# Kernel optimization log

Measured on AMD Instinct MI355X. Metric: run time of the kernel, lower is better.

The kernel has to match this reference:

```python
import jax, jax.numpy as jnp
import numpy as np

K = 3  # kernel_size, padding=1, stride=1 (same-size unfold)


def unfold3x3(x):
    """x: [B, C, H, W] -> [B, C, 9, H, W], matching torch.nn.Unfold(3, padding=1)
    channel-major / row-major kernel-position ordering."""
    H, W = x.shape[2], x.shape[3]
    xp = jnp.pad(x, ((0, 0), (0, 0), (1, 1), (1, 1)))
    patches = [xp[:, :, i:i + H, j:j + W] for i in range(K) for j in range(K)]
    return jnp.stack(patches, axis=2)


def setup_inputs() -> dict:
    key = jax.random.key(0)
    k1, k2, k3, k4 = jax.random.split(key, 4)
    B, CF, H, W = 2, 64, 64, 2048
    coord_C = 3
    out_Cs = (16, 64)  # out_Cs[-1] == CF
    features = jax.random.normal(k1, (B, CF, H, W), dtype=jnp.float32)
    coord = jax.random.normal(k2, (B, coord_C, H, W), dtype=jnp.float32)
    w0 = jax.random.normal(k3, (out_Cs[0], coord_C), dtype=jnp.float32) * 0.1
    w1 = jax.random.normal(k4, (out_Cs[1], out_Cs[0]), dtype=jnp.float32) * 0.1
    return {"features": features, "coord": coord, "w0": w0, "w1": w1}


def reference(features, coord, w0, w1):
    # --- gather 3x3 coord neighborhood, relative coords ---
    coord_sample = unfold3x3(coord)                    # [B, 3, 9, H, W]
    center = coord[:, :, None]                         # [B, 3, 1, H, W]
    rel = coord_sample - center
    rel = jnp.where(center == -1.0, 0.0, rel)          # zero invalid centers
    # --- weight-generation MLP: 1x1 convs over channel dim, per pixel & neighbor ---
    h = jnp.einsum('oc,bcnhw->bonhw', w0, rel)         # [B, 16, 9, H, W]
    h = jnp.einsum('oc,bcnhw->bonhw', w1, h)           # [B, 64, 9, H, W]
    weights = jax.nn.relu(h)                           # ReLU only after last layer
    # --- gather 3x3 feature neighborhood, weighted combine ---
    feat_sample = unfold3x3(features)                  # [B, CF, 9, H, W]
    out = feat_sample * weights                        # [B, CF, 9, H, W]
    B, CF, KK, H, W = out.shape
    return out.reshape(B, CF * KK, H, W)               # [B, CF*9, H, W]
```

## Files before the change

### kernel.cpp

```cpp
#include <hip/hip_runtime.h>

#define BB   2
#define CF_  64
#define CC   3
#define HH   64
#define WW   2048
#define HWs  (HH * WW)
#define KK   9
#define CFS  4
#define CFT  (CF_ / CFS)
#define PX   2

typedef float f2 __attribute__((ext_vector_type(2)));

__global__ __launch_bounds__(256) void fused_unfold_mlp_kernel(
    const float* __restrict__ feat,
    const float* __restrict__ coord,
    const float* __restrict__ w0,
    const float* __restrict__ w1,
    float* __restrict__ out)
{
    __shared__ float Msh[CFT * CC];

    const int t = threadIdx.x;
    const int p = blockIdx.x * 256 + t;
    const int q = p >> 17;

    if (t < CFT * CC) {
        const int o = t / CC, c = t - o * CC;
        const int og = q * CFT + o;
        float acc = 0.f;
#pragma unroll
        for (int k = 0; k < 16; k++)
            acc = fmaf(w1[og * 16 + k], w0[k * CC + c], acc);
        Msh[t] = acc;
    }
    __syncthreads();

    float ms[CFT * CC];
#pragma unroll
    for (int j = 0; j < CFT * CC; j++)
        ms[j] = __uint_as_float(__builtin_amdgcn_readfirstlane(__float_as_uint(Msh[j])));

    const int w2  = p & (WW / 2 - 1);
    const int w0p = w2 * 2;
    const int h   = (p >> 10) & (HH - 1);
    const int b   = (p >> 16) & (BB - 1);

    const float* __restrict__ cb = coord + (size_t)b * CC * HWs;
    float rel[PX][CC][KK];
#pragma unroll
    for (int px = 0; px < PX; px++) {
        const int w = w0p + px;
        float center[CC];
#pragma unroll
        for (int c = 0; c < CC; c++)
            center[c] = cb[c * HWs + h * WW + w];
#pragma unroll
        for (int n = 0; n < KK; n++) {
            const int di = n / 3 - 1, dj = n % 3 - 1;
            const int hh = h + di, ww = w + dj;
            const bool v = (hh >= 0) && (hh < HH) && (ww >= 0) && (ww < WW);
            const int off = (v ? hh : h) * WW + (v ? ww : w);
#pragma unroll
            for (int c = 0; c < CC; c++) {
                const float r = cb[c * HWs + off] - center[c];
                rel[px][c][n] = (v && center[c] != -1.0f) ? r : 0.0f;
            }
        }
    }

    int rows[3];
    rows[0] = (h > 0      ? h - 1 : 0     ) * WW;
    rows[1] = h * WW;
    rows[2] = (h < HH - 1 ? h + 1 : HH - 1) * WW;
    const int cm1 = (w0p > 0)      ? (w0p - 1) : 0;
    const int cp2 = (w0p + 2 < WW) ? (w0p + 2) : (WW - 1);

    const float* __restrict__ fb = feat + (size_t)b * CF_ * HWs;
    const int cfbase = q * CFT;
    f2* __restrict__ ob2 = (f2*)(out
        + (size_t)(b * CF_ * KK + cfbase * KK) * HWs + (size_t)h * WW + w0p);

    auto loadF = [&](float* buf, int cfi) {
        const float* fc = fb + (size_t)(cfbase + cfi) * HWs;
#pragma unroll
        for (int r = 0; r < 3; r++) {
            const float* rp = fc + rows[r];
            buf[r * 4 + 0] = rp[cm1];
            const f2 mid   = *(const f2*)(rp + w0p);
            buf[r * 4 + 1] = mid[0];
            buf[r * 4 + 2] = mid[1];
            buf[r * 4 + 3] = rp[cp2];
        }
    };

    auto computeStore = [&](const float* fv, int i) {
        const float m0 = ms[i * CC + 0], m1 = ms[i * CC + 1], m2 = ms[i * CC + 2];
#pragma unroll
        for (int n = 0; n < KK; n++) {
            const int r = n / 3, j = n % 3;
            float wg0 = fmaf(m2, rel[0][2][n],
                        fmaf(m1, rel[0][1][n], m0 * rel[0][0][n]));
            float wg1 = fmaf(m2, rel[1][2][n],
                        fmaf(m1, rel[1][1][n], m0 * rel[1][0][n]));
            f2 v;
            v[0] = fv[r * 4 + j]     * fmaxf(wg0, 0.f);
            v[1] = fv[r * 4 + j + 1] * fmaxf(wg1, 0.f);
            __builtin_nontemporal_store(v, ob2 + (size_t)(i * KK + n) * (HWs / 2));
        }
    };

    float fvA[12], fvB[12];
    loadF(fvA, 0);
#pragma unroll
    for (int i = 0; i < CFT; i += 2) {
        loadF(fvB, i + 1);
        computeStore(fvA, i);
        if (i + 2 < CFT) loadF(fvA, i + 2);
        computeStore(fvB, i + 1);
    }
}

extern "C" void kernel_launch(void* const* d_in, const int* in_sizes, int n_in,
                              void* d_out, int out_size, void* d_ws, size_t ws_size,
                              hipStream_t stream) {
    const float* feat  = (const float*)d_in[0];
    const float* coord = (const float*)d_in[1];
    const float* w0    = (const float*)d_in[2];
    const float* w1    = (const float*)d_in[3];
    float* out = (float*)d_out;

    const int total  = BB * HH * (WW / PX) * CFS;
    const int blocks = total / 256;
    fused_unfold_mlp_kernel<<<blocks, 256, 0, stream>>>(feat, coord, w0, w1, out);
}
```

Baseline: 681.0 us.

## Widen to 4 pixels per thread, remap blocks, and factor relative-coord weights algebraically

Each thread now produces 4 adjacent pixels and writes 16-byte vector stores instead of 8-byte ones. The block index is decoded into a new (h, q, wseg, b) mapping, so neighbouring blocks share rows and batches. The per-pixel relative-coordinate array is replaced by raw coordinate samples plus a precomputed center bias (weight = M·s − M·(k·center)), with invalid neighbours masked by zeroing the feature values at edges. The manual double-buffered feature load is replaced by a simple unroll-4 loop, which trades explicit prefetch for compiler scheduling and raises register pressure.

```diff
diff --git a/kernel.cpp b/kernel.cpp
--- a/kernel.cpp
+++ b/kernel.cpp
@@ -9,9 +9,9 @@
 #define KK   9
 #define CFS  4
 #define CFT  (CF_ / CFS)
-#define PX   2
+#define PX   4
 
-typedef float f2 __attribute__((ext_vector_type(2)));
+typedef float f4 __attribute__((ext_vector_type(4)));
 
 __global__ __launch_bounds__(256) void fused_unfold_mlp_kernel(
     const float* __restrict__ feat,
@@ -22,9 +22,15 @@
 {
     __shared__ float Msh[CFT * CC];
 
-    const int t = threadIdx.x;
-    const int p = blockIdx.x * 256 + t;
-    const int q = p >> 17;
+    const int t  = threadIdx.x;
+    const int id   = blockIdx.x;
+    const int cl   = id >> 7;
+    const int hw   = (id >> 4) & 7;
+    const int q    = (id >> 2) & 3;
+    const int wseg = (id >> 1) & 1;
+    const int b    = id & 1;
+    const int h    = cl * 8 + hw;
+    const int w0p  = (wseg * 256 + t) * PX;
 
     if (t < CFT * CC) {
         const int o = t / CC, c = t - o * CC;
@@ -42,83 +48,94 @@
     for (int j = 0; j < CFT * CC; j++)
         ms[j] = __uint_as_float(__builtin_amdgcn_readfirstlane(__float_as_uint(Msh[j])));
 
-    const int w2  = p & (WW / 2 - 1);
-    const int w0p = w2 * 2;
-    const int h   = (p >> 10) & (HH - 1);
-    const int b   = (p >> 16) & (BB - 1);
-
-    const float* __restrict__ cb = coord + (size_t)b * CC * HWs;
-    float rel[PX][CC][KK];
-#pragma unroll
-    for (int px = 0; px < PX; px++) {
-        const int w = w0p + px;
-        float center[CC];
-#pragma unroll
-        for (int c = 0; c < CC; c++)
-            center[c] = cb[c * HWs + h * WW + w];
-#pragma unroll
-        for (int n = 0; n < KK; n++) {
-            const int di = n / 3 - 1, dj = n % 3 - 1;
-            const int hh = h + di, ww = w + dj;
-            const bool v = (hh >= 0) && (hh < HH) && (ww >= 0) && (ww < WW);
-            const int off = (v ? hh : h) * WW + (v ? ww : w);
-#pragma unroll
-            for (int c = 0; c < CC; c++) {
-                const float r = cb[c * HWs + off] - center[c];
-                rel[px][c][n] = (v && center[c] != -1.0f) ? r : 0.0f;
-            }
-        }
-    }
-
     int rows[3];
     rows[0] = (h > 0      ? h - 1 : 0     ) * WW;
     rows[1] = h * WW;
     rows[2] = (h < HH - 1 ? h + 1 : HH - 1) * WW;
-    const int cm1 = (w0p > 0)      ? (w0p - 1) : 0;
-    const int cp2 = (w0p + 2 < WW) ? (w0p + 2) : (WW - 1);
+    const int cm1 = (w0p > 0)       ? (w0p - 1)  : 0;
+    const int cp4 = (w0p + PX < WW) ? (w0p + PX) : (WW - 1);
+
+    const float* __restrict__ cb = coord + (size_t)b * CC * HWs;
+    float mc[CC][PX];
+    float kf[CC][PX];
+    float s[CC][3][PX + 2];
+#pragma unroll
+    for (int c = 0; c < CC; c++) {
+        const float* cc = cb + (size_t)c * HWs;
+        const f4 ctr = *(const f4*)(cc + rows[1] + w0p);
+#pragma unroll
+        for (int px = 0; px < PX; px++) {
+            const float k = (ctr[px] != -1.0f) ? 1.0f : 0.0f;
+            kf[c][px] = k;
+            mc[c][px] = k * ctr[px];
+        }
+#pragma unroll
+        for (int r = 0; r < 3; r++) {
+            const float* rp = cc + rows[r];
+            s[c][r][0] = rp[cm1];
+            const f4 mid = *(const f4*)(rp + w0p);
+#pragma unroll
+            for (int px = 0; px < PX; px++) s[c][r][1 + px] = mid[px];
+            s[c][r][5] = rp[cp4];
+        }
+    }
+
+    const bool edge = (h == 0) | (h == HH - 1) | (w0p == 0) | (w0p + PX == WW);
+    const float vR0 = (h > 0)       ? 1.f : 0.f;
+    const float vR2 = (h < HH - 1)  ? 1.f : 0.f;
+    const float vCl = (w0p > 0)     ? 1.f : 0.f;
+    const float vCr = (w0p + PX < WW) ? 1.f : 0.f;
 
     const float* __restrict__ fb = feat + (size_t)b * CF_ * HWs;
     const int cfbase = q * CFT;
-    f2* __restrict__ ob2 = (f2*)(out
-        + (size_t)(b * CF_ * KK + cfbase * KK) * HWs + (size_t)h * WW + w0p);
+    f4* __restrict__ ob4 = (f4*)(out
+        + (size_t)(b * CF_ + cfbase) * KK * HWs + (size_t)h * WW + w0p);
 
-    auto loadF = [&](float* buf, int cfi) {
-        const float* fc = fb + (size_t)(cfbase + cfi) * HWs;
+#pragma unroll 4
+    for (int i = 0; i < CFT; i++) {
+        const float* fc = fb + (size_t)(cfbase + i) * HWs;
+        float ft[3][PX + 2];
 #pragma unroll
         for (int r = 0; r < 3; r++) {
             const float* rp = fc + rows[r];
-            buf[r * 4 + 0] = rp[cm1];
-            const f2 mid   = *(const f2*)(rp + w0p);
-            buf[r * 4 + 1] = mid[0];
-            buf[r * 4 + 2] = mid[1];
-            buf[r * 4 + 3] = rp[cp2];
+            ft[r][0] = rp[cm1];
+            const f4 mid = *(const f4*)(rp + w0p);
+#pragma unroll
+            for (int px = 0; px < PX; px++) ft[r][1 + px] = mid[px];
+            ft[r][5] = rp[cp4];
         }
-    };
+        if (edge) {
+            ft[0][0] *= vR0 * vCl; ft[0][5] *= vR0 * vCr;
+            ft[2][0] *= vR2 * vCl; ft[2][5] *= vR2 * vCr;
+            ft[1][0] *= vCl;       ft[1][5] *= vCr;
+#pragma unroll
+            for (int jj = 1; jj < 5; jj++) { ft[0][jj] *= vR0; ft[2][jj] *= vR2; }
+        }
 
-    auto computeStore = [&](const float* fv, int i) {
         const float m0 = ms[i * CC + 0], m1 = ms[i * CC + 1], m2 = ms[i * CC + 2];
+        float mk[CC][PX], bb[PX];
+#pragma unroll
+        for (int px = 0; px < PX; px++) {
+            mk[0][px] = m0 * kf[0][px];
+            mk[1][px] = m1 * kf[1][px];
+            mk[2][px] = m2 * kf[2][px];
+            bb[px] = fmaf(m2, mc[2][px], fmaf(m1, mc[1][px], m0 * mc[0][px]));
+        }
+
 #pragma unroll
         for (int n = 0; n < KK; n++) {
             const int r = n / 3, j = n % 3;
-            float wg0 = fmaf(m2, rel[0][2][n],
-                        fmaf(m1, rel[0][1][n], m0 * rel[0][0][n]));
-            float wg1 = fmaf(m2, rel[1][2][n],
-                        fmaf(m1, rel[1][1][n], m0 * rel[1][0][n]));
-            f2 v;
-            v[0] = fv[r * 4 + j]     * fmaxf(wg0, 0.f);
-            v[1] = fv[r * 4 + j + 1] * fmaxf(wg1, 0.f);
-            __builtin_nontemporal_store(v, ob2 + (size_t)(i * KK + n) * (HWs / 2));
+            f4 v;
+#pragma unroll
+            for (int px = 0; px < PX; px++) {
+                const int jj = px + j;
+                float wgt = fmaf(mk[0][px], s[0][r][jj],
+                            fmaf(mk[1][px], s[1][r][jj],
+                            fmaf(mk[2][px], s[2][r][jj], -bb[px])));
+                v[px] = ft[r][jj] * fmaxf(wgt, 0.0f);
+            }
+            __builtin_nontemporal_store(v, ob4 + (size_t)(i * KK + n) * (HWs / PX));
         }
-    };
-
-    float fvA[12], fvB[12];
-    loadF(fvA, 0);
-#pragma unroll
-    for (int i = 0; i < CFT; i += 2) {
-        loadF(fvB, i + 1);
-        computeStore(fvA, i);
-        if (i + 2 < CFT) loadF(fvA, i + 2);
-        computeStore(fvB, i + 1);
     }
 }
 
```

New measurement: 712.9 us. 4.7% more time.

## Map one block per feature-channel row with float4 windows and folded weight algebra

Applied to the files above, without the earlier changes.

Remaps the work so each 512-thread block handles one full image row for one (batch, feature channel), with each thread covering four adjacent pixels and using float4 loads and stores. The relative-coordinate MLP is folded into a masked per-pixel affine form, weight = mk·neighbor − mk·center, which removes the per-neighbor subtraction and the separate relative-coordinate array. Border handling moves from clamped scalar gathers to clamped vector windows plus zero masks on the feature values. The aim is wider, fully contiguous output stores and less indexing work. The cost is that the coordinate rows are reloaded for every feature channel instead of being shared across 16 channels per thread, which adds load traffic that should mostly hit in cache.

```diff
diff --git a/kernel.cpp b/kernel.cpp
--- a/kernel.cpp
+++ b/kernel.cpp
@@ -7,119 +7,99 @@
 #define WW   2048
 #define HWs  (HH * WW)
 #define KK   9
-#define CFS  4
-#define CFT  (CF_ / CFS)
-#define PX   2
+#define TPB  512
 
-typedef float f2 __attribute__((ext_vector_type(2)));
+typedef float f4 __attribute__((ext_vector_type(4)));
 
-__global__ __launch_bounds__(256) void fused_unfold_mlp_kernel(
+__global__ __launch_bounds__(TPB, 4) void fused_unfold_mlp_kernel(
     const float* __restrict__ feat,
     const float* __restrict__ coord,
     const float* __restrict__ w0,
     const float* __restrict__ w1,
     float* __restrict__ out)
 {
-    __shared__ float Msh[CFT * CC];
+    const int t  = threadIdx.x;
+    const int id = blockIdx.x;
+    const int h  = id & (HH - 1);
+    const int cf = (id >> 6) & (CF_ - 1);
+    const int b  = id >> 12;
 
-    const int t = threadIdx.x;
-    const int p = blockIdx.x * 256 + t;
-    const int q = p >> 17;
-
-    if (t < CFT * CC) {
-        const int o = t / CC, c = t - o * CC;
-        const int og = q * CFT + o;
+    float m[CC];
+#pragma unroll
+    for (int c = 0; c < CC; c++) {
         float acc = 0.f;
 #pragma unroll
         for (int k = 0; k < 16; k++)
-            acc = fmaf(w1[og * 16 + k], w0[k * CC + c], acc);
-        Msh[t] = acc;
+            acc = fmaf(w1[cf * 16 + k], w0[k * CC + c], acc);
+        m[c] = __uint_as_float(__builtin_amdgcn_readfirstlane(__float_as_uint(acc)));
     }
-    __syncthreads();
 
-    float ms[CFT * CC];
-#pragma unroll
-    for (int j = 0; j < CFT * CC; j++)
-        ms[j] = __uint_as_float(__builtin_amdgcn_readfirstlane(__float_as_uint(Msh[j])));
+    const int g  = t * 4;
+    const int bL = (g >= 4) ? (g - 4) : 0;
+    const int bR = (g + 4 <= WW - 4) ? (g + 4) : (WW - 4);
+    const bool eL = (t == 0), eR = (t == TPB - 1);
 
-    const int w2  = p & (WW / 2 - 1);
-    const int w0p = w2 * 2;
-    const int h   = (p >> 10) & (HH - 1);
-    const int b   = (p >> 16) & (BB - 1);
+    const int r0 = (h > 0      ? h - 1 : 0     ) * WW;
+    const int r1 = h * WW;
+    const int r2 = (h < HH - 1 ? h + 1 : HH - 1) * WW;
+    const float rm0 = (h > 0)      ? 1.f : 0.f;
+    const float rm2 = (h < HH - 1) ? 1.f : 0.f;
 
     const float* __restrict__ cb = coord + (size_t)b * CC * HWs;
-    float rel[PX][CC][KK];
+    const float* __restrict__ fr = feat  + ((size_t)b * CF_ + cf) * HWs;
+    float* __restrict__ ob = out + (size_t)(b * CF_ + cf) * KK * HWs
+                                 + (size_t)h * WW + g;
+
+    float mk[CC][4], bb[4];
+
+    auto ldwin = [&](const float* base, float* w) {
+        *(f4*)(w)     = *(const f4*)(base + bL);
+        *(f4*)(w + 4) = *(const f4*)(base + g);
+        *(f4*)(w + 8) = *(const f4*)(base + bR);
+    };
+
+    auto doRow = [&](int ro, float rm, int n0, bool isCenter) {
+        float cw[CC][12], fw[12];
 #pragma unroll
-    for (int px = 0; px < PX; px++) {
-        const int w = w0p + px;
-        float center[CC];
+        for (int c = 0; c < CC; c++) ldwin(cb + (size_t)c * HWs + ro, cw[c]);
+        ldwin(fr + ro, fw);
+
+        if (isCenter) {
 #pragma unroll
-        for (int c = 0; c < CC; c++)
-            center[c] = cb[c * HWs + h * WW + w];
+            for (int px = 0; px < 4; px++) {
+                float acc = 0.f;
 #pragma unroll
-        for (int n = 0; n < KK; n++) {
-            const int di = n / 3 - 1, dj = n % 3 - 1;
-            const int hh = h + di, ww = w + dj;
-            const bool v = (hh >= 0) && (hh < HH) && (ww >= 0) && (ww < WW);
-            const int off = (v ? hh : h) * WW + (v ? ww : w);
-#pragma unroll
-            for (int c = 0; c < CC; c++) {
-                const float r = cb[c * HWs + off] - center[c];
-                rel[px][c][n] = (v && center[c] != -1.0f) ? r : 0.0f;
+                for (int c = 0; c < CC; c++) {
+                    const float cen = cw[c][4 + px];
+                    const float kk  = (cen != -1.0f) ? 1.f : 0.f;
+                    mk[c][px] = m[c] * kk;
+                    acc = fmaf(mk[c][px], cen, acc);
+                }
+                bb[px] = acc;
             }
         }
-    }
 
-    int rows[3];
-    rows[0] = (h > 0      ? h - 1 : 0     ) * WW;
-    rows[1] = h * WW;
-    rows[2] = (h < HH - 1 ? h + 1 : HH - 1) * WW;
-    const int cm1 = (w0p > 0)      ? (w0p - 1) : 0;
-    const int cp2 = (w0p + 2 < WW) ? (w0p + 2) : (WW - 1);
-
-    const float* __restrict__ fb = feat + (size_t)b * CF_ * HWs;
-    const int cfbase = q * CFT;
-    f2* __restrict__ ob2 = (f2*)(out
-        + (size_t)(b * CF_ * KK + cfbase * KK) * HWs + (size_t)h * WW + w0p);
-
-    auto loadF = [&](float* buf, int cfi) {
-        const float* fc = fb + (size_t)(cfbase + cfi) * HWs;
 #pragma unroll
-        for (int r = 0; r < 3; r++) {
-            const float* rp = fc + rows[r];
-            buf[r * 4 + 0] = rp[cm1];
-            const f2 mid   = *(const f2*)(rp + w0p);
-            buf[r * 4 + 1] = mid[0];
-            buf[r * 4 + 2] = mid[1];
-            buf[r * 4 + 3] = rp[cp2];
+        for (int j = 0; j < 3; j++) {
+            f4 v;
+#pragma unroll
+            for (int px = 0; px < 4; px++) {
+                const int idx = 4 + px + j - 1;
+                float wgt = fmaf(mk[2][px], cw[2][idx],
+                            fmaf(mk[1][px], cw[1][idx],
+                            fmaf(mk[0][px], cw[0][idx], -bb[px])));
+                float ft = fw[idx];
+                if (px == 0 && j == 0) ft = eL ? 0.f : ft;
+                if (px == 3 && j == 2) ft = eR ? 0.f : ft;
+                v[px] = ft * rm * fmaxf(wgt, 0.f);
+            }
+            __builtin_nontemporal_store(v, (f4*)(ob + (size_t)(n0 + j) * HWs));
         }
     };
 
-    auto computeStore = [&](const float* fv, int i) {
-        const float m0 = ms[i * CC + 0], m1 = ms[i * CC + 1], m2 = ms[i * CC + 2];
-#pragma unroll
-        for (int n = 0; n < KK; n++) {
-            const int r = n / 3, j = n % 3;
-            float wg0 = fmaf(m2, rel[0][2][n],
-                        fmaf(m1, rel[0][1][n], m0 * rel[0][0][n]));
-            float wg1 = fmaf(m2, rel[1][2][n],
-                        fmaf(m1, rel[1][1][n], m0 * rel[1][0][n]));
-            f2 v;
-            v[0] = fv[r * 4 + j]     * fmaxf(wg0, 0.f);
-            v[1] = fv[r * 4 + j + 1] * fmaxf(wg1, 0.f);
-            __builtin_nontemporal_store(v, ob2 + (size_t)(i * KK + n) * (HWs / 2));
-        }
-    };
-
-    float fvA[12], fvB[12];
-    loadF(fvA, 0);
-#pragma unroll
-    for (int i = 0; i < CFT; i += 2) {
-        loadF(fvB, i + 1);
-        computeStore(fvA, i);
-        if (i + 2 < CFT) loadF(fvA, i + 2);
-        computeStore(fvB, i + 1);
-    }
+    doRow(r1, 1.f, 3, true);
+    doRow(r0, rm0, 0, false);
+    doRow(r2, rm2, 6, false);
 }
 
 extern "C" void kernel_launch(void* const* d_in, const int* in_sizes, int n_in,
@@ -131,7 +111,6 @@
     const float* w1    = (const float*)d_in[3];
     float* out = (float*)d_out;
 
-    const int total  = BB * HH * (WW / PX) * CFS;
-    const int blocks = total / 256;
-    fused_unfold_mlp_kernel<<<blocks, 256, 0, stream>>>(feat, coord, w0, w1, out);
+    const int blocks = BB * CF_ * HH;
+    fused_unfold_mlp_kernel<<<blocks, TPB, 0, stream>>>(feat, coord, w0, w1, out);
 }
```

Measured after the change: 727.8 us. +6.9%, slower.
